# Kernel optimization log

Measured on AMD Instinct MI355X. Metric: run time of the kernel, lower is better.

## Reference

```python
import jax, jax.numpy as jnp
import numpy as np

EPS = 1e-6

def _rmsnorm(x, w):
    # matches RMSNorm: compute in fp32, cast back, then scale by weight
    dt = x.dtype
    xf = x.astype(jnp.float32)
    var = jnp.mean(xf * xf, axis=-1, keepdims=True)
    xf = xf * jax.lax.rsqrt(var + EPS)
    return xf.astype(dt) * w


def setup_inputs() -> dict:
    key = jax.random.key(0)
    ks = jax.random.split(key, 4)
    B, N, C = 4, 2048, 1024
    H = 16
    D = C // H
    x = jax.random.normal(ks[0], (B, N, C), dtype=jnp.float32)
    W_qkv = jax.random.normal(ks[1], (C, 3 * C), dtype=jnp.float32) * (1.0 / np.sqrt(C))
    b_qkv = jnp.zeros((3 * C,), dtype=jnp.float32)
    W_proj = jax.random.normal(ks[2], (C, C), dtype=jnp.float32) * (1.0 / np.sqrt(C))
    b_proj = jnp.zeros((C,), dtype=jnp.float32)
    qn_w = jnp.ones((D,), dtype=jnp.float32)
    kn_w = jnp.ones((D,), dtype=jnp.float32)
    return {"x": x, "W_qkv": W_qkv, "b_qkv": b_qkv, "W_proj": W_proj,
            "b_proj": b_proj, "qn_w": qn_w, "kn_w": kn_w}


def reference(x, W_qkv, b_qkv, W_proj, b_proj, qn_w, kn_w):
    B, N, C = x.shape
    H = 16
    D = C // H
    qkv = jnp.einsum('bnc,cd->bnd', x, W_qkv) + b_qkv          # [B,N,3C]
    qkv = qkv.reshape(B, N, 3, H, D)
    q = qkv[:, :, 0].transpose(0, 2, 1, 3)                     # [B,H,N,D]
    k = qkv[:, :, 1].transpose(0, 2, 1, 3)
    v = qkv[:, :, 2].transpose(0, 2, 1, 3)
    q = _rmsnorm(q, qn_w)
    k = _rmsnorm(k, kn_w)
    scale = D ** -0.5
    attn = jnp.einsum('bhqd,bhkd->bhqk', q, k) * scale         # [B,H,N,N]
    attn = jax.nn.softmax(attn, axis=-1)
    out = jnp.einsum('bhqk,bhkd->bhqd', attn, v)               # [B,H,N,D]
    out = out.transpose(0, 2, 1, 3).reshape(B, N, C)
    out = jnp.einsum('bnc,cd->bnd', out, W_proj) + b_proj
    return out
```

## Files before the change

### kernel.cpp

```cpp
#include <hip/hip_runtime.h>
#include <stdint.h>

#define B_ 4
#define N_ 2048
#define C_ 1024
#define H_ 16
#define D_ 64
#define M_ (B_*N_)
#define N3_ (3*C_)

typedef __attribute__((ext_vector_type(8))) __bf16 bf16x8;
typedef bf16x8 bf16x8_ma __attribute__((may_alias));
typedef __attribute__((ext_vector_type(4))) float floatx4;
typedef unsigned short u16;
typedef unsigned int u32;

typedef __attribute__((address_space(1))) const void void_g;
typedef __attribute__((address_space(3))) void void_l;

__device__ __forceinline__ void glds16(const void* g, void* l) {
  __builtin_amdgcn_global_load_lds((void_g*)g, (void_l*)l, 16, 0, 0);
}

__device__ __forceinline__ u16 f2bf(float f) {
  union { float f; u32 u; } x; x.f = f;
  u32 r = x.u + 0x7fffu + ((x.u >> 16) & 1u);
  return (u16)(r >> 16);
}

__device__ __forceinline__ float fexp2(float x) {
#if __has_builtin(__builtin_amdgcn_exp2f)
  return __builtin_amdgcn_exp2f(x);
#else
  return exp2f(x);
#endif
}

__global__ __launch_bounds__(256)
void convert_x(const float4* __restrict__ in, uint2* __restrict__ out, int n4) {
  int idx = blockIdx.x * 256 + threadIdx.x;
  if (idx >= n4) return;
  float4 v = in[idx];
  union { u16 a[4]; uint2 u; } p;
  p.a[0] = f2bf(v.x); p.a[1] = f2bf(v.y); p.a[2] = f2bf(v.z); p.a[3] = f2bf(v.w);
  out[idx] = p.u;
}

__global__ __launch_bounds__(256)
void transpose_cvt(const float* __restrict__ in, u16* __restrict__ out,
                   int R, int Ccols) {
  __shared__ u16 tile[64][65];
  int c0 = blockIdx.x * 64, r0 = blockIdx.y * 64;
  int tid = threadIdx.x;
#pragma unroll
  for (int it = 0; it < 16; ++it) {
    int idx = it * 256 + tid;
    int r = idx >> 6, c = idx & 63;
    tile[c][r] = f2bf(in[(size_t)(r0 + r) * Ccols + c0 + c]);
  }
  __syncthreads();
#pragma unroll
  for (int it = 0; it < 16; ++it) {
    int idx = it * 256 + tid;
    int oc = idx >> 6, orr = idx & 63;
    out[(size_t)(c0 + oc) * R + r0 + orr] = tile[oc][orr];
  }
}

__global__ __launch_bounds__(256)
void transpose_v(const u16* __restrict__ qkv, u16* __restrict__ vt) {
  __shared__ u16 tile[64][65];
  int bh = blockIdx.y, b = bh >> 4, h = bh & 15;
  int n0 = blockIdx.x * 64;
  int tid = threadIdx.x;
#pragma unroll
  for (int it = 0; it < 16; ++it) {
    int idx = it * 256 + tid;
    int n = idx >> 6, d = idx & 63;
    tile[d][n] = qkv[(size_t)(b * N_ + n0 + n) * N3_ + 2 * C_ + h * D_ + d];
  }
  __syncthreads();
#pragma unroll
  for (int it = 0; it < 16; ++it) {
    int idx = it * 256 + tid;
    int d = idx >> 6, n = idx & 63;
    int np = (n & 0x23) | ((n & 0x0C) << 1) | ((n & 0x10) >> 2);
    vt[(size_t)(bh * D_ + d) * N_ + n0 + np] = tile[d][n];
  }
}

__global__ __launch_bounds__(256)
void gemm_bt(const u16* __restrict__ A, const u16* __restrict__ Bt,
             const float* __restrict__ bias, void* __restrict__ Cout,
             int Ncols, int lda, int do_rms, int out_fp32,
             const float* __restrict__ qn, const float* __restrict__ kn) {
  __shared__ __align__(16) u16 sA[3][8 * 512];
  __shared__ __align__(16) u16 sB[3][8 * 512];
  const int K = C_;
  int tid = threadIdx.x;
  int wave = tid >> 6, lane = tid & 63;
  int lrow = lane & 15, lq = lane >> 4;
  int n0 = blockIdx.x * 128;
  int m0 = blockIdx.y * 128;
  int wm = wave >> 1, wn = wave & 1;

  floatx4 acc[4][4];
#pragma unroll
  for (int i = 0; i < 4; ++i)
#pragma unroll
    for (int j = 0; j < 4; ++j) acc[i][j] = (floatx4){0.f, 0.f, 0.f, 0.f};

  const u16* ga0 = A  + (size_t)(m0 + (2 * wave + 0) * 16 + lrow) * lda + lq * 8;
  const u16* ga1 = A  + (size_t)(m0 + (2 * wave + 1) * 16 + lrow) * lda + lq * 8;
  const u16* gb0 = Bt + (size_t)(n0 + (2 * wave + 0) * 16 + lrow) * K + lq * 8;
  const u16* gb1 = Bt + (size_t)(n0 + (2 * wave + 1) * 16 + lrow) * K + lq * 8;
  int o0 = (2 * wave + 0) * 512;
  int o1 = (2 * wave + 1) * 512;

  u16* aA = &sA[0][0]; u16* aB = &sA[1][0]; u16* aC = &sA[2][0];
  u16* bA = &sB[0][0]; u16* bB = &sB[1][0]; u16* bC = &sB[2][0];

  glds16(ga0, aA + o0); glds16(ga1, aA + o1);
  glds16(gb0, bA + o0); glds16(gb1, bA + o1);
  glds16(ga0 + 32, aB + o0); glds16(ga1 + 32, aB + o1);
  glds16(gb0 + 32, bB + o0); glds16(gb1 + 32, bB + o1);

  for (int kt = 0; kt < K; kt += 32) {
    if (kt + 32 < K) {
      asm volatile("s_waitcnt vmcnt(4)" ::: "memory");
    } else {
      asm volatile("s_waitcnt vmcnt(0)" ::: "memory");
    }
    __builtin_amdgcn_s_barrier();
    asm volatile("" ::: "memory");

    if (kt + 64 < K) {
      glds16(ga0 + kt + 64, aC + o0);
      glds16(ga1 + kt + 64, aC + o1);
      glds16(gb0 + kt + 64, bC + o0);
      glds16(gb1 + kt + 64, bC + o1);
    }

    bf16x8 af[4], bfr[4];
#pragma unroll
    for (int i = 0; i < 4; ++i)
      af[i] = *(const bf16x8_ma*)(aA + (wm * 4 + i) * 512 + lane * 8);
#pragma unroll
    for (int j = 0; j < 4; ++j)
      bfr[j] = *(const bf16x8_ma*)(bA + (wn * 4 + j) * 512 + lane * 8);
#pragma unroll
    for (int i = 0; i < 4; ++i)
#pragma unroll
      for (int j = 0; j < 4; ++j)
        acc[i][j] = __builtin_amdgcn_mfma_f32_16x16x32_bf16(af[i], bfr[j], acc[i][j], 0, 0, 0);

    u16* t;
    t = aA; aA = aB; aB = aC; aC = t;
    t = bA; bA = bB; bB = bC; bC = t;
  }

  int colbase = n0 + wn * 64;
  float bv[4];
#pragma unroll
  for (int j = 0; j < 4; ++j) bv[j] = bias[colbase + j * 16 + lrow];
#pragma unroll
  for (int i = 0; i < 4; ++i)
#pragma unroll
    for (int j = 0; j < 4; ++j)
#pragma unroll
      for (int r = 0; r < 4; ++r) acc[i][j][r] += bv[j];

  int sect = colbase >> 10;
  if (do_rms && sect < 2) {
    const float* wptr = (sect == 0) ? qn : kn;
    float wv[4];
#pragma unroll
    for (int j = 0; j < 4; ++j) wv[j] = wptr[j * 16 + lrow];
#pragma unroll
    for (int i = 0; i < 4; ++i)
#pragma unroll
      for (int r = 0; r < 4; ++r) {
        float ss = 0.f;
#pragma unroll
        for (int j = 0; j < 4; ++j) { float v = acc[i][j][r]; ss += v * v; }
        ss += __shfl_xor(ss, 1);
        ss += __shfl_xor(ss, 2);
        ss += __shfl_xor(ss, 4);
        ss += __shfl_xor(ss, 8);
        float rstd = rsqrtf(ss * (1.0f / 64.0f) + 1e-6f);
#pragma unroll
        for (int j = 0; j < 4; ++j) acc[i][j][r] *= rstd * wv[j];
      }
  }

#pragma unroll
  for (int i = 0; i < 4; ++i)
#pragma unroll
    for (int j = 0; j < 4; ++j)
#pragma unroll
      for (int r = 0; r < 4; ++r) {
        int row = m0 + wm * 64 + i * 16 + lq * 4 + r;
        int col = colbase + j * 16 + lrow;
        if (out_fp32)
          ((float*)Cout)[(size_t)row * Ncols + col] = acc[i][j][r];
        else
          ((u16*)Cout)[(size_t)row * Ncols + col] = f2bf(acc[i][j][r]);
      }
}

__global__ __launch_bounds__(256)
void flash_attn(u16* __restrict__ qkv, const u16* __restrict__ vt) {
  __shared__ __align__(16) u16 sK[2][8 * 512];
  __shared__ __align__(16) u16 sV[2][8 * 512];
  int tid = threadIdx.x;
  int wave = tid >> 6, lane = tid & 63;
  int lrow = lane & 15, lq = lane >> 4;
  int bh = blockIdx.y, b = bh >> 4, h = bh & 15;
  int q0 = blockIdx.x * 128;
  const float cc = 0.125f * 1.44269504088896340736f;
  const float co = 8.5f * 1.44269504088896340736f;

  bf16x8 qf[2][2];
#pragma unroll
  for (int i = 0; i < 2; ++i)
#pragma unroll
    for (int kq = 0; kq < 2; ++kq)
      qf[i][kq] = *(const bf16x8_ma*)(qkv +
          (size_t)(b * N_ + q0 + wave * 32 + i * 16 + lrow) * N3_ +
          h * D_ + kq * 32 + lq * 8);

  union { bf16x8 v; u16 e[8]; } one_;
#pragma unroll
  for (int e = 0; e < 8; ++e) one_.e[e] = 0x3F80;
  bf16x8 onef = one_.v;

  floatx4 aco[2][4];
  floatx4 acl[2];
#pragma unroll
  for (int i = 0; i < 2; ++i) {
#pragma unroll
    for (int nd = 0; nd < 4; ++nd) aco[i][nd] = (floatx4){0.f, 0.f, 0.f, 0.f};
    acl[i] = (floatx4){0.f, 0.f, 0.f, 0.f};
  }

  const u16* gk[2];
  const u16* gv[2];
#pragma unroll
  for (int t = 0; t < 2; ++t) {
    int blk = wave * 2 + t;
    int j = blk >> 1, kq = blk & 1;
    gk[t] = qkv + (size_t)(b * N_ + j * 16 + lrow) * N3_ +
            C_ + h * D_ + kq * 32 + lq * 8;
    gv[t] = vt + (size_t)(bh * D_ + j * 16 + lrow) * N_ + kq * 32 + lq * 8;
  }

  u16* k_cur = &sK[0][0]; u16* k_nxt = &sK[1][0];
  u16* v_cur = &sV[0][0]; u16* v_nxt = &sV[1][0];

#pragma unroll
  for (int t = 0; t < 2; ++t) {
    int blk = wave * 2 + t;
    glds16(gk[t], k_cur + blk * 512);
    glds16(gv[t], v_cur + blk * 512);
  }
  __syncthreads();

  for (int kt = 0; kt < 32; ++kt) {
    if (kt < 31) {
      size_t key0n = (size_t)(kt + 1) * 64;
#pragma unroll
      for (int t = 0; t < 2; ++t) {
        int blk = wave * 2 + t;
        glds16(gk[t] + key0n * N3_, k_nxt + blk * 512);
        glds16(gv[t] + key0n, v_nxt + blk * 512);
      }
    }

    floatx4 accs[2][4];
    __builtin_amdgcn_s_setprio(1);
#pragma unroll
    for (int j = 0; j < 4; ++j) {
      bf16x8 kf0 = *(const bf16x8_ma*)(k_cur + (j * 2 + 0) * 512 + lane * 8);
      bf16x8 kf1 = *(const bf16x8_ma*)(k_cur + (j * 2 + 1) * 512 + lane * 8);
#pragma unroll
      for (int i = 0; i < 2; ++i) {
        floatx4 s = (floatx4){0.f, 0.f, 0.f, 0.f};
        s = __builtin_amdgcn_mfma_f32_16x16x32_bf16(kf0, qf[i][0], s, 0, 0, 0);
        s = __builtin_amdgcn_mfma_f32_16x16x32_bf16(kf1, qf[i][1], s, 0, 0, 0);
        accs[i][j] = s;
      }
    }
    __builtin_amdgcn_s_setprio(0);

    bf16x8 pf[2][2];
#pragma unroll
    for (int i = 0; i < 2; ++i) {
      union { bf16x8 v; __bf16 e[8]; } pk0, pk1;
#pragma unroll
      for (int j = 0; j < 4; ++j)
#pragma unroll
        for (int r = 0; r < 4; ++r) {
          float p = fexp2(fmaf(accs[i][j][r], cc, -co));
          if (j < 2) pk0.e[(j & 1) * 4 + r] = (__bf16)p;
          else       pk1.e[(j & 1) * 4 + r] = (__bf16)p;
        }
      pf[i][0] = pk0.v;
      pf[i][1] = pk1.v;
    }

    __builtin_amdgcn_s_setprio(1);
#pragma unroll
    for (int kq = 0; kq < 2; ++kq) {
#pragma unroll
      for (int nd = 0; nd < 4; ++nd) {
        bf16x8 vf = *(const bf16x8_ma*)(v_cur + (nd * 2 + kq) * 512 + lane * 8);
        aco[0][nd] = __builtin_amdgcn_mfma_f32_16x16x32_bf16(vf, pf[0][kq], aco[0][nd], 0, 0, 0);
        aco[1][nd] = __builtin_amdgcn_mfma_f32_16x16x32_bf16(vf, pf[1][kq], aco[1][nd], 0, 0, 0);
      }
      acl[0] = __builtin_amdgcn_mfma_f32_16x16x32_bf16(onef, pf[0][kq], acl[0], 0, 0, 0);
      acl[1] = __builtin_amdgcn_mfma_f32_16x16x32_bf16(onef, pf[1][kq], acl[1], 0, 0, 0);
    }
    __builtin_amdgcn_s_setprio(0);

    __syncthreads();
    u16* t0 = k_cur; k_cur = k_nxt; k_nxt = t0;
    u16* t1 = v_cur; v_cur = v_nxt; v_nxt = t1;
  }

#pragma unroll
  for (int i = 0; i < 2; ++i) {
    float inv = 1.0f / acl[i][0];
    int row = q0 + wave * 32 + i * 16 + lrow;
#pragma unroll
    for (int nd = 0; nd < 4; ++nd) {
      union { u16 a[4]; uint2 u; } st;
#pragma unroll
      for (int r = 0; r < 4; ++r) st.a[r] = f2bf(aco[i][nd][r] * inv);
      *(uint2*)(qkv + (size_t)(b * N_ + row) * N3_ + h * D_ + nd * 16 + lq * 4) = st.u;
    }
  }
}

extern "C" void kernel_launch(void* const* d_in, const int* in_sizes, int n_in,
                              void* d_out, int out_size, void* d_ws, size_t ws_size,
                              hipStream_t stream) {
  (void)in_sizes; (void)n_in; (void)out_size; (void)ws_size;
  const float* x     = (const float*)d_in[0];
  const float* Wqkv  = (const float*)d_in[1];
  const float* bqkv  = (const float*)d_in[2];
  const float* Wproj = (const float*)d_in[3];
  const float* bproj = (const float*)d_in[4];
  const float* qn    = (const float*)d_in[5];
  const float* kn    = (const float*)d_in[6];
  float* out = (float*)d_out;

  char* ws = (char*)d_ws;
  u16* xb      = (u16*)ws;  ws += (size_t)M_ * C_ * 2;
  u16* Wt_qkv  = (u16*)ws;  ws += (size_t)N3_ * C_ * 2;
  u16* Wt_proj = (u16*)ws;  ws += (size_t)C_ * C_ * 2;
  u16* qkv     = (u16*)ws;  ws += (size_t)M_ * N3_ * 2;
  u16* vt      = (u16*)ws;  ws += (size_t)B_ * H_ * D_ * N_ * 2;

  convert_x<<<dim3(M_ * C_ / 4 / 256), 256, 0, stream>>>(
      (const float4*)x, (uint2*)xb, M_ * C_ / 4);
  transpose_cvt<<<dim3(N3_ / 64, C_ / 64), 256, 0, stream>>>(Wqkv, Wt_qkv, C_, N3_);
  transpose_cvt<<<dim3(C_ / 64, C_ / 64), 256, 0, stream>>>(Wproj, Wt_proj, C_, C_);
  gemm_bt<<<dim3(N3_ / 128, M_ / 128), 256, 0, stream>>>(
      xb, Wt_qkv, bqkv, qkv, N3_, C_, 1, 0, qn, kn);
  transpose_v<<<dim3(N_ / 64, B_ * H_), 256, 0, stream>>>(qkv, vt);
  flash_attn<<<dim3(N_ / 128, B_ * H_), 256, 0, stream>>>(qkv, vt);
  gemm_bt<<<dim3(C_ / 128, M_ / 128), 256, 0, stream>>>(
      qkv, Wt_proj, bproj, out, C_, N3_, 0, 1, qn, kn);
}
```

Baseline: 341.9 us.

## Add 256x256 tiled QKV GEMM with deeper pipeline and prescale Q in attention

Replaces the 128x128 QKV projection GEMM with a 512-thread 256x256 tile kernel using a four-stage LDS pipeline and fused bias plus QK RMSNorm epilogue, raising arithmetic intensity per loaded byte. Flash attention now multiplies Q by the softmax scale once at load and removes the per-element fma and fixed offset before exp2. Risks: larger LDS footprint limits occupancy and 384 blocks quantize poorly over CUs; prescaling Q in bf16 adds rounding.

```diff
diff --git a/kernel.cpp b/kernel.cpp
--- a/kernel.cpp
+++ b/kernel.cpp
@@ -87,6 +87,118 @@
     int np = (n & 0x23) | ((n & 0x0C) << 1) | ((n & 0x10) >> 2);
     vt[(size_t)(bh * D_ + d) * N_ + n0 + np] = tile[d][n];
   }
+}
+
+__global__ __launch_bounds__(512, 2)
+void gemm_qkv_256(const u16* __restrict__ A, const u16* __restrict__ Bt,
+                  const float* __restrict__ bias, u16* __restrict__ Cout,
+                  const float* __restrict__ qn, const float* __restrict__ kn) {
+  __shared__ __align__(16) u16 sA[4][16 * 512];
+  __shared__ __align__(16) u16 sB[4][16 * 512];
+  const int K = C_;
+  int tid = threadIdx.x;
+  int wave = tid >> 6, lane = tid & 63;
+  int lrow = lane & 15, lq = lane >> 4;
+  int n0 = blockIdx.x * 256;
+  int m0 = blockIdx.y * 256;
+  int wm = wave >> 2, wn = wave & 3;
+
+  floatx4 acc[8][4];
+#pragma unroll
+  for (int i = 0; i < 8; ++i)
+#pragma unroll
+    for (int j = 0; j < 4; ++j) acc[i][j] = (floatx4){0.f, 0.f, 0.f, 0.f};
+
+  const u16* pa0 = A  + (size_t)(m0 + (2 * wave + 0) * 16 + lrow) * K + lq * 8;
+  const u16* pa1 = A  + (size_t)(m0 + (2 * wave + 1) * 16 + lrow) * K + lq * 8;
+  const u16* pb0 = Bt + (size_t)(n0 + (2 * wave + 0) * 16 + lrow) * K + lq * 8;
+  const u16* pb1 = Bt + (size_t)(n0 + (2 * wave + 1) * 16 + lrow) * K + lq * 8;
+  int oa0 = (2 * wave + 0) * 512, oa1 = (2 * wave + 1) * 512;
+
+#define STAGE_HK(hk_)                                   \
+  do {                                                  \
+    int s_ = (hk_) & 3;                                 \
+    int ko_ = (hk_) * 32;                               \
+    glds16(pa0 + ko_, &sA[s_][oa0]);                    \
+    glds16(pa1 + ko_, &sA[s_][oa1]);                    \
+    glds16(pb0 + ko_, &sB[s_][oa0]);                    \
+    glds16(pb1 + ko_, &sB[s_][oa1]);                    \
+  } while (0)
+
+  STAGE_HK(0); STAGE_HK(1); STAGE_HK(2);
+
+  for (int hk = 0; hk < 32; ++hk) {
+    if (hk < 30)       asm volatile("s_waitcnt vmcnt(8)" ::: "memory");
+    else if (hk == 30) asm volatile("s_waitcnt vmcnt(4)" ::: "memory");
+    else               asm volatile("s_waitcnt vmcnt(0)" ::: "memory");
+    __builtin_amdgcn_s_barrier();
+    asm volatile("" ::: "memory");
+
+    if (hk + 3 < 32) STAGE_HK(hk + 3);
+
+    int s = hk & 3;
+    bf16x8 af[8], bfr[4];
+#pragma unroll
+    for (int i = 0; i < 8; ++i)
+      af[i] = *(const bf16x8_ma*)(&sA[s][(wm * 8 + i) * 512 + lane * 8]);
+#pragma unroll
+    for (int j = 0; j < 4; ++j)
+      bfr[j] = *(const bf16x8_ma*)(&sB[s][(wn * 4 + j) * 512 + lane * 8]);
+
+    __builtin_amdgcn_s_setprio(1);
+#pragma unroll
+    for (int i = 0; i < 8; ++i)
+#pragma unroll
+      for (int j = 0; j < 4; ++j)
+        acc[i][j] = __builtin_amdgcn_mfma_f32_16x16x32_bf16(af[i], bfr[j], acc[i][j], 0, 0, 0);
+    __builtin_amdgcn_s_setprio(0);
+  }
+#undef STAGE_HK
+
+  int colbase = n0 + wn * 64;
+  float bv[4];
+#pragma unroll
+  for (int j = 0; j < 4; ++j) bv[j] = bias[colbase + j * 16 + lrow];
+#pragma unroll
+  for (int i = 0; i < 8; ++i)
+#pragma unroll
+    for (int j = 0; j < 4; ++j)
+#pragma unroll
+      for (int r = 0; r < 4; ++r) acc[i][j][r] += bv[j];
+
+  int sect = colbase >> 10;
+  if (sect < 2) {
+    const float* wptr = (sect == 0) ? qn : kn;
+    float wv[4];
+#pragma unroll
+    for (int j = 0; j < 4; ++j) wv[j] = wptr[j * 16 + lrow];
+#pragma unroll
+    for (int i = 0; i < 8; ++i)
+#pragma unroll
+      for (int r = 0; r < 4; ++r) {
+        float ss = 0.f;
+#pragma unroll
+        for (int j = 0; j < 4; ++j) { float v = acc[i][j][r]; ss += v * v; }
+        ss += __shfl_xor(ss, 1);
+        ss += __shfl_xor(ss, 2);
+        ss += __shfl_xor(ss, 4);
+        ss += __shfl_xor(ss, 8);
+        float rstd = rsqrtf(ss * (1.0f / 64.0f) + 1e-6f);
+#pragma unroll
+        for (int j = 0; j < 4; ++j) acc[i][j][r] *= rstd * wv[j];
+      }
+  }
+
+#pragma unroll
+  for (int i = 0; i < 8; ++i)
+#pragma unroll
+    for (int j = 0; j < 4; ++j)
+#pragma unroll
+      for (int r = 0; r < 4; ++r) {
+        int row = m0 + wm * 128 + i * 16 + lq * 4 + r;
+        int col = colbase + j * 16 + lrow;
+        Cout[(size_t)row * N3_ + col] = f2bf(acc[i][j][r]);
+      }
 }
 
 __global__ __launch_bounds__(256)
@@ -218,16 +330,20 @@
   int bh = blockIdx.y, b = bh >> 4, h = bh & 15;
   int q0 = blockIdx.x * 128;
   const float cc = 0.125f * 1.44269504088896340736f;
-  const float co = 8.5f * 1.44269504088896340736f;
 
   bf16x8 qf[2][2];
 #pragma unroll
   for (int i = 0; i < 2; ++i)
 #pragma unroll
-    for (int kq = 0; kq < 2; ++kq)
-      qf[i][kq] = *(const bf16x8_ma*)(qkv +
+    for (int kq = 0; kq < 2; ++kq) {
+      union { bf16x8 v; __bf16 e[8]; } t;
+      t.v = *(const bf16x8_ma*)(qkv +
           (size_t)(b * N_ + q0 + wave * 32 + i * 16 + lrow) * N3_ +
           h * D_ + kq * 32 + lq * 8);
+#pragma unroll
+      for (int e = 0; e < 8; ++e) t.e[e] = (__bf16)((float)t.e[e] * cc);
+      qf[i][kq] = t.v;
+    }
 
   union { bf16x8 v; u16 e[8]; } one_;
 #pragma unroll
@@ -300,7 +416,7 @@
       for (int j = 0; j < 4; ++j)
 #pragma unroll
         for (int r = 0; r < 4; ++r) {
-          float p = fexp2(fmaf(accs[i][j][r], cc, -co));
+          float p = fexp2(accs[i][j][r]);
           if (j < 2) pk0.e[(j & 1) * 4 + r] = (__bf16)p;
           else       pk1.e[(j & 1) * 4 + r] = (__bf16)p;
         }
@@ -365,8 +481,8 @@
       (const float4*)x, (uint2*)xb, M_ * C_ / 4);
   transpose_cvt<<<dim3(N3_ / 64, C_ / 64), 256, 0, stream>>>(Wqkv, Wt_qkv, C_, N3_);
   transpose_cvt<<<dim3(C_ / 64, C_ / 64), 256, 0, stream>>>(Wproj, Wt_proj, C_, C_);
-  gemm_bt<<<dim3(N3_ / 128, M_ / 128), 256, 0, stream>>>(
-      xb, Wt_qkv, bqkv, qkv, N3_, C_, 1, 0, qn, kn);
+  gemm_qkv_256<<<dim3(N3_ / 256, M_ / 256), 512, 0, stream>>>(
+      xb, Wt_qkv, bqkv, qkv, qn, kn);
   transpose_v<<<dim3(N_ / 64, B_ * H_), 256, 0, stream>>>(qkv, vt);
   flash_attn<<<dim3(N_ / 128, B_ * H_), 256, 0, stream>>>(qkv, vt);
   gemm_bt<<<dim3(C_ / 128, M_ / 128), 256, 0, stream>>>(
```

Result: no change. 340.1 us (-0.5%).
